# Performance work log

Measured on AMD Instinct MI355X. Metric: run time of the kernel, lower is better.

Reference implementation:

```python
import jax, jax.numpy as jnp
import numpy as np

# Model dims (match init_kwargs / input_specs)
B, CIN, COUT = 32, 32, 64
H, W = 128, 128
KH, KW = 3, 3
MAXCN = 64                    # max entries in connect_nums_list
HO, WO = H - KH + 1, W - KW + 1   # padding=0, stride=1


def setup_inputs() -> dict:
    key = jax.random.key(0)
    k1, k2, k3, k4 = jax.random.split(key, 4)
    x = jax.random.normal(k1, (B, CIN, H, W), dtype=jnp.float32)
    # padded kernel bank: [out_channel, connection_slot, kh, kw]
    weights = jax.random.normal(k2, (COUT, MAXCN, KH, KW), dtype=jnp.float32)
    # per-pixel bias map per output channel (original inits zeros; random exercises it)
    bias = jax.random.normal(k3, (COUT, HO, WO), dtype=jnp.float32) * 0.1
    connect_nums = jax.random.randint(k4, (COUT,), 1, MAXCN + 1, dtype=jnp.int32)
    return {"x": x, "weights": weights, "bias": bias, "connect_nums": connect_nums}


def reference(x, weights, bias, connect_nums):
    O, J = weights.shape[0], weights.shape[1]
    # mask out kernel slots beyond each channel's connection count
    mask = (jnp.arange(J)[None, :] < connect_nums[:, None]).astype(weights.dtype)  # [O,J]
    # slot j reads input channel j % CIN; conv is linear, so fold duplicate-channel
    # kernels into one effective dense kernel [O, CIN, KH, KW]
    onehot = jax.nn.one_hot(jnp.arange(J) % CIN, CIN, dtype=weights.dtype)  # [J,C]
    kdense = jnp.einsum('ojhw,oj,jc->ochw', weights, mask, onehot)
    out = jax.lax.conv_general_dilated(
        x, kdense, window_strides=(1, 1), padding='VALID',
        dimension_numbers=('NCHW', 'OIHW', 'NCHW'))  # [B,O,HO,WO]
    return out + bias[None]
```

## Files before the change

### kernel.cpp

```cpp
#include <hip/hip_runtime.h>

#define B_    32
#define CIN   32
#define COUT  64
#define H_    128
#define W_    128
#define HO_   126
#define WO_   126
#define MAXCN 64

typedef __attribute__((ext_vector_type(8))) short short8;
typedef __attribute__((ext_vector_type(4))) float floatx4;

static __device__ __forceinline__ unsigned short f2bf(float f) {
    union { float f; unsigned u; } v; v.f = f;
    unsigned r = v.u + 0x7fff + ((v.u >> 16) & 1);
    return (unsigned short)(r >> 16);
}

__global__ void fold_bf16(const float* __restrict__ w,
                          const int* __restrict__ cn,
                          unsigned short* __restrict__ wk) {
    int idx = blockIdx.x * 256 + threadIdx.x;
    if (idx >= 9 * COUT * CIN) return;
    int c   = idx & 31;
    int oc  = (idx >> 5) & 63;
    int tap = idx >> 11;
    int n = cn[oc];
    float v = 0.0f;
    if (c < n)      v += w[(oc * MAXCN + c) * 9 + tap];
    if (c + 32 < n) v += w[(oc * MAXCN + c + 32) * 9 + tap];
    wk[((tap * 4 + (c >> 3)) * 64 + oc) * 8 + (c & 7)] = f2bf(v);
}

__global__ __launch_bounds__(256)
void nchw_to_nhwc_bf16(const float* __restrict__ x,
                       unsigned short* __restrict__ xb) {
    const int b = blockIdx.y, y = blockIdx.x;
    const int t = threadIdx.x;
    const int c8  = t & 3;
    const int xi0 = t >> 2;
    const float* xp = x + (size_t)b * CIN * H_ * W_ + (size_t)y * W_;
#pragma unroll
    for (int it = 0; it < 2; ++it) {
        const int xi = xi0 + it * 64;
        __align__(16) unsigned short v[8];
#pragma unroll
        for (int j = 0; j < 8; ++j) {
            const int c = c8 * 8 + j;
            v[j] = f2bf(xp[(size_t)c * (H_ * W_) + xi]);
        }
        *(uint4*)(xb + (((size_t)b * H_ + y) * W_ + xi) * CIN + c8 * 8) =
            *(const uint4*)v;
    }
}

__global__ __launch_bounds__(256)
void bias_to_nhwc(const float* __restrict__ bias, float* __restrict__ bn) {
    int idx = blockIdx.x * 256 + threadIdx.x;
    int oc = idx & 63;
    int p  = idx >> 6;
    int y  = p / WO_;
    int x  = p - y * WO_;
    bn[idx] = bias[((size_t)oc * HO_ + y) * WO_ + x];
}

__global__ __launch_bounds__(256, 4)
void conv_mfma(const unsigned short* __restrict__ xb,
               const unsigned short* __restrict__ wk,
               const float* __restrict__ bnhwc,
               float* __restrict__ out) {
    const int strip = blockIdx.x;
    const int yseg  = blockIdx.y;
    const int img   = blockIdx.z;
    const int tid  = threadIdx.x;
    const int w_id = tid >> 6, lane = tid & 63;
    const int quad = lane >> 4, l16 = lane & 15;
    const int ocg  = w_id & 1;
    const int rseg = w_id >> 1;
    const int x0    = strip * 16;
    const int ybase = yseg * 16 + rseg * 8;
    const int col   = x0 + l16;
    const int colb  = col > (W_ - 3) ? (W_ - 3) : col;

    const short8* wq8 = (const short8*)wk;
    short8 a[9][2];
#pragma unroll
    for (int tap = 0; tap < 9; ++tap)
#pragma unroll
        for (int t = 0; t < 2; ++t)
            a[tap][t] = wq8[(tap * 4 + quad) * 64 + ocg * 32 + t * 16 + l16];

    const unsigned short* xbi = xb + (size_t)img * (H_ * W_ * CIN);
    float* ob = out + ((size_t)img * COUT + ocg * 32) * (HO_ * WO_);

    const int nit = (HO_ - ybase) < 8 ? (HO_ - ybase) : 8;

    for (int it = 0; it < nit; ++it) {
        const int y = ybase + it;

        const int colc = col > (WO_ - 1) ? (WO_ - 1) : col;
        const float* bp = bnhwc + ((size_t)y * WO_ + colc) * COUT + ocg * 32 + quad * 4;
        floatx4 acc[2];
        {
            const float4 b0 = *(const float4*)(bp);
            const float4 b1 = *(const float4*)(bp + 16);
            acc[0] = floatx4{b0.x, b0.y, b0.z, b0.w};
            acc[1] = floatx4{b1.x, b1.y, b1.z, b1.w};
        }

#pragma unroll
        for (int r = 0; r < 3; ++r) {
            const unsigned short* prow =
                xbi + ((size_t)(y + r) * W_ + colb) * CIN + quad * 8;
            const short8 b0 = *(const short8*)(prow);
            const short8 b1 = *(const short8*)(prow + CIN);
            const short8 b2 = *(const short8*)(prow + 2 * CIN);
            acc[0] = __builtin_amdgcn_mfma_f32_16x16x32_bf16(a[r * 3 + 0][0], b0, acc[0], 0, 0, 0);
            acc[1] = __builtin_amdgcn_mfma_f32_16x16x32_bf16(a[r * 3 + 0][1], b0, acc[1], 0, 0, 0);
            acc[0] = __builtin_amdgcn_mfma_f32_16x16x32_bf16(a[r * 3 + 1][0], b1, acc[0], 0, 0, 0);
            acc[1] = __builtin_amdgcn_mfma_f32_16x16x32_bf16(a[r * 3 + 1][1], b1, acc[1], 0, 0, 0);
            acc[0] = __builtin_amdgcn_mfma_f32_16x16x32_bf16(a[r * 3 + 2][0], b2, acc[0], 0, 0, 0);
            acc[1] = __builtin_amdgcn_mfma_f32_16x16x32_bf16(a[r * 3 + 2][1], b2, acc[1], 0, 0, 0);
        }

        if (col < WO_) {
#pragma unroll
            for (int t = 0; t < 2; ++t)
#pragma unroll
                for (int r4 = 0; r4 < 4; ++r4) {
                    const int oc_l = t * 16 + quad * 4 + r4;
                    ob[((size_t)oc_l * HO_ + y) * WO_ + col] = acc[t][r4];
                }
        }
    }
}

__global__ void fold_kernel(const float* __restrict__ w,
                            const int* __restrict__ cn,
                            float* __restrict__ kd) {
    int idx = blockIdx.x * blockDim.x + threadIdx.x;
    if (idx >= COUT * CIN * 9) return;
    int t = idx % 9;
    int c = (idx / 9) % CIN;
    int o = idx / (9 * CIN);
    int n = cn[o];
    float v = 0.0f;
    if (c < n)      v += w[(o * MAXCN + c) * 9 + t];
    if (c + 32 < n) v += w[(o * MAXCN + c + 32) * 9 + t];
    kd[idx] = v;
}

__global__ __launch_bounds__(256)
void conv_kernel(const float* __restrict__ x,
                 const float* __restrict__ kd,
                 const float* __restrict__ bias,
                 float* __restrict__ out) {
    __shared__ __align__(16) float xsh[CIN * 18 * 20];
    __shared__ __align__(16) float wsh[16 * 289];
    const int b = blockIdx.z, ocg = blockIdx.y, tile = blockIdx.x;
    const int ty = tile >> 3, txx = tile & 7;
    const int y0 = ty * 16, x0 = txx * 16;
    const int tid = threadIdx.x;
    const float* xbp = x + (size_t)b * CIN * H_ * W_;
    for (int idx = tid; idx < CIN * 18 * 18; idx += 256) {
        int c = idx / 324, rem = idx - c * 324, r = rem / 18, col = rem - r * 18;
        int iy = y0 + r;   if (iy > H_ - 1) iy = H_ - 1;
        int ix = x0 + col; if (ix > W_ - 1) ix = W_ - 1;
        xsh[c * 360 + r * 20 + col] = xbp[(c * H_ + iy) * W_ + ix];
    }
    for (int idx = tid; idx < 16 * 288; idx += 256) {
        int oc = idx / 288, rr = idx - oc * 288;
        wsh[oc * 289 + rr] = kd[(ocg * 16 + oc) * 288 + rr];
    }
    __syncthreads();
    const int oc_l = tid & 15, pb = tid >> 4, pby = pb >> 2, pbx = pb & 3;
    float acc[4][4];
#pragma unroll
    for (int i = 0; i < 4; ++i)
#pragma unroll
        for (int j = 0; j < 4; ++j) acc[i][j] = 0.0f;
    const float* xp = &xsh[(pby * 4) * 20 + pbx * 4];
    const float* wp = &wsh[oc_l * 289];
    for (int c = 0; c < CIN; ++c) {
        float xr[6][6];
#pragma unroll
        for (int r = 0; r < 6; ++r) {
            const float* row = xp + c * 360 + r * 20;
            float4 v4 = *reinterpret_cast<const float4*>(row);
            float2 v2 = *reinterpret_cast<const float2*>(row + 4);
            xr[r][0] = v4.x; xr[r][1] = v4.y; xr[r][2] = v4.z;
            xr[r][3] = v4.w; xr[r][4] = v2.x; xr[r][5] = v2.y;
        }
        float wr[9];
#pragma unroll
        for (int t = 0; t < 9; ++t) wr[t] = wp[c * 9 + t];
#pragma unroll
        for (int kh = 0; kh < 3; ++kh)
#pragma unroll
            for (int kw = 0; kw < 3; ++kw) {
                const float wv = wr[kh * 3 + kw];
#pragma unroll
                for (int i = 0; i < 4; ++i)
#pragma unroll
                    for (int j = 0; j < 4; ++j)
                        acc[i][j] = fmaf(xr[i + kh][j + kw], wv, acc[i][j]);
            }
    }
    const int o = ocg * 16 + oc_l;
    const int yb = y0 + pby * 4, xq0 = x0 + pbx * 4;
    float* ob = out + ((size_t)(b * COUT + o)) * HO_ * WO_;
    const float* bb = bias + (size_t)o * HO_ * WO_;
#pragma unroll
    for (int i = 0; i < 4; ++i) {
        int y = yb + i;
        if (y >= HO_) continue;
#pragma unroll
        for (int j = 0; j < 4; ++j) {
            int xq = xq0 + j;
            if (xq >= WO_) continue;
            ob[y * WO_ + xq] = acc[i][j] + bb[y * WO_ + xq];
        }
    }
}

extern "C" void kernel_launch(void* const* d_in, const int* in_sizes, int n_in,
                              void* d_out, int out_size, void* d_ws, size_t ws_size,
                              hipStream_t stream) {
    const float* x    = (const float*)d_in[0];
    const float* w    = (const float*)d_in[1];
    const float* bias = (const float*)d_in[2];
    const int*   cn   = (const int*)d_in[3];
    float* out = (float*)d_out;

    const size_t XB_BYTES = (size_t)B_ * H_ * W_ * CIN * 2;
    const size_t WK_BYTES = (size_t)9 * COUT * CIN * 2;
    const size_t BN_BYTES = (size_t)HO_ * WO_ * COUT * 4;

    if (ws_size >= XB_BYTES + WK_BYTES + BN_BYTES) {
        unsigned short* xbuf = (unsigned short*)d_ws;
        unsigned short* wkb  = (unsigned short*)((char*)d_ws + XB_BYTES);
        float*          bnb  = (float*)((char*)d_ws + XB_BYTES + WK_BYTES);
        fold_bf16<<<72, 256, 0, stream>>>(w, cn, wkb);
        nchw_to_nhwc_bf16<<<dim3(H_, B_), 256, 0, stream>>>(x, xbuf);
        bias_to_nhwc<<<3969, 256, 0, stream>>>(bias, bnb);
        conv_mfma<<<dim3(8, 8, B_), 256, 0, stream>>>(xbuf, wkb, bnb, out);
    } else {
        float* kd = (float*)d_ws;
        fold_kernel<<<(COUT * CIN * 9 + 255) / 256, 256, 0, stream>>>(w, cn, kd);
        dim3 grid(64, 4, B_);
        conv_kernel<<<grid, 256, 0, stream>>>(x, kd, bias, out);
    }
}
```

Measured before the change: 288.2 us.

## Reuse input rows across output rows via rolling register window; merge prep kernels

In the conv kernel, each wave now keeps a rolling window of 4 input rows in registers, so every new output row loads only one new input row instead of three. This cuts redundant global loads by roughly 3x in the main path, and the loop is fully unrolled. Separately, the weight-fold and bias-transpose kernels are merged into one launch, and the occupancy hint is lowered from 4 to 3 to leave room for the extra registers. The cost is higher register pressure, less latency hiding from occupancy, and a duplicated fallback path for partial segments.

```diff
diff --git a/kernel.cpp b/kernel.cpp
--- a/kernel.cpp
+++ b/kernel.cpp
@@ -18,19 +18,30 @@
     return (unsigned short)(r >> 16);
 }
 
-__global__ void fold_bf16(const float* __restrict__ w,
-                          const int* __restrict__ cn,
-                          unsigned short* __restrict__ wk) {
-    int idx = blockIdx.x * 256 + threadIdx.x;
-    if (idx >= 9 * COUT * CIN) return;
-    int c   = idx & 31;
-    int oc  = (idx >> 5) & 63;
-    int tap = idx >> 11;
-    int n = cn[oc];
-    float v = 0.0f;
-    if (c < n)      v += w[(oc * MAXCN + c) * 9 + tap];
-    if (c + 32 < n) v += w[(oc * MAXCN + c + 32) * 9 + tap];
-    wk[((tap * 4 + (c >> 3)) * 64 + oc) * 8 + (c & 7)] = f2bf(v);
+__global__ __launch_bounds__(256)
+void prep(const float* __restrict__ w, const int* __restrict__ cn,
+          unsigned short* __restrict__ wk,
+          const float* __restrict__ bias, float* __restrict__ bn) {
+    const int bid = blockIdx.x;
+    if (bid < 72) {
+        int idx = bid * 256 + threadIdx.x;
+        if (idx >= 9 * COUT * CIN) return;
+        int c   = idx & 31;
+        int oc  = (idx >> 5) & 63;
+        int tap = idx >> 11;
+        int n = cn[oc];
+        float v = 0.0f;
+        if (c < n)      v += w[(oc * MAXCN + c) * 9 + tap];
+        if (c + 32 < n) v += w[(oc * MAXCN + c + 32) * 9 + tap];
+        wk[((tap * 4 + (c >> 3)) * 64 + oc) * 8 + (c & 7)] = f2bf(v);
+    } else {
+        int idx = (bid - 72) * 256 + threadIdx.x;
+        int oc = idx & 63;
+        int p  = idx >> 6;
+        int y  = p / WO_;
+        int x  = p - y * WO_;
+        bn[idx] = bias[((size_t)oc * HO_ + y) * WO_ + x];
+    }
 }
 
 __global__ __launch_bounds__(256)
@@ -55,17 +66,7 @@
     }
 }
 
-__global__ __launch_bounds__(256)
-void bias_to_nhwc(const float* __restrict__ bias, float* __restrict__ bn) {
-    int idx = blockIdx.x * 256 + threadIdx.x;
-    int oc = idx & 63;
-    int p  = idx >> 6;
-    int y  = p / WO_;
-    int x  = p - y * WO_;
-    bn[idx] = bias[((size_t)oc * HO_ + y) * WO_ + x];
-}
-
-__global__ __launch_bounds__(256, 4)
+__global__ __launch_bounds__(256, 3)
 void conv_mfma(const unsigned short* __restrict__ xb,
                const unsigned short* __restrict__ wk,
                const float* __restrict__ bnhwc,
@@ -82,6 +83,7 @@
     const int ybase = yseg * 16 + rseg * 8;
     const int col   = x0 + l16;
     const int colb  = col > (W_ - 3) ? (W_ - 3) : col;
+    const int colc  = col > (WO_ - 1) ? (WO_ - 1) : col;
 
     const short8* wq8 = (const short8*)wk;
     short8 a[9][2];
@@ -90,48 +92,92 @@
 #pragma unroll
         for (int t = 0; t < 2; ++t)
             a[tap][t] = wq8[(tap * 4 + quad) * 64 + ocg * 32 + t * 16 + l16];
+#pragma unroll
+    for (int tap = 0; tap < 9; ++tap)
+#pragma unroll
+        for (int t = 0; t < 2; ++t)
+            asm volatile("" : "+v"(a[tap][t]));
 
     const unsigned short* xbi = xb + (size_t)img * (H_ * W_ * CIN);
     float* ob = out + ((size_t)img * COUT + ocg * 32) * (HO_ * WO_);
 
     const int nit = (HO_ - ybase) < 8 ? (HO_ - ybase) : 8;
 
-    for (int it = 0; it < nit; ++it) {
-        const int y = ybase + it;
-
-        const int colc = col > (WO_ - 1) ? (WO_ - 1) : col;
-        const float* bp = bnhwc + ((size_t)y * WO_ + colc) * COUT + ocg * 32 + quad * 4;
-        floatx4 acc[2];
-        {
+    if (nit == 8) {
+        short8 bw[4][3];
+#pragma unroll
+        for (int r = 0; r < 3; ++r) {
+            const unsigned short* prow =
+                xbi + ((size_t)(ybase + r) * W_ + colb) * CIN + quad * 8;
+            bw[r][0] = *(const short8*)(prow);
+            bw[r][1] = *(const short8*)(prow + CIN);
+            bw[r][2] = *(const short8*)(prow + 2 * CIN);
+        }
+#pragma unroll
+        for (int it = 0; it < 8; ++it) {
+            const int y = ybase + it;
+            if (it < 7) {
+                const unsigned short* prow =
+                    xbi + ((size_t)(y + 3) * W_ + colb) * CIN + quad * 8;
+                const int s = (it + 3) & 3;
+                bw[s][0] = *(const short8*)(prow);
+                bw[s][1] = *(const short8*)(prow + CIN);
+                bw[s][2] = *(const short8*)(prow + 2 * CIN);
+            }
+            const float* bp = bnhwc + ((size_t)y * WO_ + colc) * COUT + ocg * 32 + quad * 4;
             const float4 b0 = *(const float4*)(bp);
             const float4 b1 = *(const float4*)(bp + 16);
-            acc[0] = floatx4{b0.x, b0.y, b0.z, b0.w};
-            acc[1] = floatx4{b1.x, b1.y, b1.z, b1.w};
-        }
-
-#pragma unroll
-        for (int r = 0; r < 3; ++r) {
-            const unsigned short* prow =
-                xbi + ((size_t)(y + r) * W_ + colb) * CIN + quad * 8;
-            const short8 b0 = *(const short8*)(prow);
-            const short8 b1 = *(const short8*)(prow + CIN);
-            const short8 b2 = *(const short8*)(prow + 2 * CIN);
-            acc[0] = __builtin_amdgcn_mfma_f32_16x16x32_bf16(a[r * 3 + 0][0], b0, acc[0], 0, 0, 0);
-            acc[1] = __builtin_amdgcn_mfma_f32_16x16x32_bf16(a[r * 3 + 0][1], b0, acc[1], 0, 0, 0);
-            acc[0] = __builtin_amdgcn_mfma_f32_16x16x32_bf16(a[r * 3 + 1][0], b1, acc[0], 0, 0, 0);
-            acc[1] = __builtin_amdgcn_mfma_f32_16x16x32_bf16(a[r * 3 + 1][1], b1, acc[1], 0, 0, 0);
-            acc[0] = __builtin_amdgcn_mfma_f32_16x16x32_bf16(a[r * 3 + 2][0], b2, acc[0], 0, 0, 0);
-            acc[1] = __builtin_amdgcn_mfma_f32_16x16x32_bf16(a[r * 3 + 2][1], b2, acc[1], 0, 0, 0);
-        }
-
-        if (col < WO_) {
-#pragma unroll
-            for (int t = 0; t < 2; ++t)
+            floatx4 acc0 = floatx4{b0.x, b0.y, b0.z, b0.w};
+            floatx4 acc1 = floatx4{b1.x, b1.y, b1.z, b1.w};
+#pragma unroll
+            for (int r = 0; r < 3; ++r) {
+                const int s = (it + r) & 3;
+                acc0 = __builtin_amdgcn_mfma_f32_16x16x32_bf16(a[r * 3 + 0][0], bw[s][0], acc0, 0, 0, 0);
+                acc1 = __builtin_amdgcn_mfma_f32_16x16x32_bf16(a[r * 3 + 0][1], bw[s][0], acc1, 0, 0, 0);
+                acc0 = __builtin_amdgcn_mfma_f32_16x16x32_bf16(a[r * 3 + 1][0], bw[s][1], acc0, 0, 0, 0);
+                acc1 = __builtin_amdgcn_mfma_f32_16x16x32_bf16(a[r * 3 + 1][1], bw[s][1], acc1, 0, 0, 0);
+                acc0 = __builtin_amdgcn_mfma_f32_16x16x32_bf16(a[r * 3 + 2][0], bw[s][2], acc0, 0, 0, 0);
+                acc1 = __builtin_amdgcn_mfma_f32_16x16x32_bf16(a[r * 3 + 2][1], bw[s][2], acc1, 0, 0, 0);
+            }
+            if (col < WO_) {
 #pragma unroll
                 for (int r4 = 0; r4 < 4; ++r4) {
-                    const int oc_l = t * 16 + quad * 4 + r4;
-                    ob[((size_t)oc_l * HO_ + y) * WO_ + col] = acc[t][r4];
+                    const int o0 = quad * 4 + r4;
+                    ob[((size_t)o0 * HO_ + y) * WO_ + col] = acc0[r4];
+                    ob[((size_t)(16 + o0) * HO_ + y) * WO_ + col] = acc1[r4];
                 }
+            }
+        }
+    } else {
+        for (int it = 0; it < nit; ++it) {
+            const int y = ybase + it;
+            const float* bp = bnhwc + ((size_t)y * WO_ + colc) * COUT + ocg * 32 + quad * 4;
+            const float4 b0 = *(const float4*)(bp);
+            const float4 b1 = *(const float4*)(bp + 16);
+            floatx4 acc0 = floatx4{b0.x, b0.y, b0.z, b0.w};
+            floatx4 acc1 = floatx4{b1.x, b1.y, b1.z, b1.w};
+#pragma unroll
+            for (int r = 0; r < 3; ++r) {
+                const unsigned short* prow =
+                    xbi + ((size_t)(y + r) * W_ + colb) * CIN + quad * 8;
+                const short8 v0 = *(const short8*)(prow);
+                const short8 v1 = *(const short8*)(prow + CIN);
+                const short8 v2 = *(const short8*)(prow + 2 * CIN);
+                acc0 = __builtin_amdgcn_mfma_f32_16x16x32_bf16(a[r * 3 + 0][0], v0, acc0, 0, 0, 0);
+                acc1 = __builtin_amdgcn_mfma_f32_16x16x32_bf16(a[r * 3 + 0][1], v0, acc1, 0, 0, 0);
+                acc0 = __builtin_amdgcn_mfma_f32_16x16x32_bf16(a[r * 3 + 1][0], v1, acc0, 0, 0, 0);
+                acc1 = __builtin_amdgcn_mfma_f32_16x16x32_bf16(a[r * 3 + 1][1], v1, acc1, 0, 0, 0);
+                acc0 = __builtin_amdgcn_mfma_f32_16x16x32_bf16(a[r * 3 + 2][0], v2, acc0, 0, 0, 0);
+                acc1 = __builtin_amdgcn_mfma_f32_16x16x32_bf16(a[r * 3 + 2][1], v2, acc1, 0, 0, 0);
+            }
+            if (col < WO_) {
+#pragma unroll
+                for (int r4 = 0; r4 < 4; ++r4) {
+                    const int o0 = quad * 4 + r4;
+                    ob[((size_t)o0 * HO_ + y) * WO_ + col] = acc0[r4];
+                    ob[((size_t)(16 + o0) * HO_ + y) * WO_ + col] = acc1[r4];
+                }
+            }
         }
     }
 }
@@ -241,9 +287,8 @@
         unsigned short* xbuf = (unsigned short*)d_ws;
         unsigned short* wkb  = (unsigned short*)((char*)d_ws + XB_BYTES);
         float*          bnb  = (float*)((char*)d_ws + XB_BYTES + WK_BYTES);
-        fold_bf16<<<72, 256, 0, stream>>>(w, cn, wkb);
+        prep<<<72 + 3969, 256, 0, stream>>>(w, cn, wkb, bias, bnb);
         nchw_to_nhwc_bf16<<<dim3(H_, B_), 256, 0, stream>>>(x, xbuf);
-        bias_to_nhwc<<<3969, 256, 0, stream>>>(bias, bnb);
         conv_mfma<<<dim3(8, 8, B_), 256, 0, stream>>>(xbuf, wkb, bnb, out);
     } else {
         float* kd = (float*)d_ws;
```

Result: faster. 279.8 us (-2.9%).

## Swap MFMA operands so output lanes run along x, drop bias transpose kernel

Applied to the files above, without the earlier changes.

The MFMA operands are swapped so that pixels form the A operand and weights the B operand. Each lane's accumulator now covers 4 consecutive output x positions for a single output channel, which allows vectorized float4 stores straight into NCHW output and float4 bias loads from the original NCHW bias. This removes the separate bias_to_nhwc kernel and its workspace buffer. Blocks now cover 32x16 output tiles with 16 channels per wave, and the tile origin is clamped at the edges, so overlapping edge tiles recompute and rewrite some pixels and take a float2 path when unaligned.

```diff
diff --git a/kernel.cpp b/kernel.cpp
--- a/kernel.cpp
+++ b/kernel.cpp
@@ -56,82 +56,75 @@
 }
 
 __global__ __launch_bounds__(256)
-void bias_to_nhwc(const float* __restrict__ bias, float* __restrict__ bn) {
-    int idx = blockIdx.x * 256 + threadIdx.x;
-    int oc = idx & 63;
-    int p  = idx >> 6;
-    int y  = p / WO_;
-    int x  = p - y * WO_;
-    bn[idx] = bias[((size_t)oc * HO_ + y) * WO_ + x];
-}
-
-__global__ __launch_bounds__(256, 4)
 void conv_mfma(const unsigned short* __restrict__ xb,
                const unsigned short* __restrict__ wk,
-               const float* __restrict__ bnhwc,
+               const float* __restrict__ bias,
                float* __restrict__ out) {
     const int strip = blockIdx.x;
     const int yseg  = blockIdx.y;
     const int img   = blockIdx.z;
+    int x0 = strip * 32; if (x0 > 94) x0 = 94;
+    int y0 = yseg * 16;  if (y0 > 110) y0 = 110;
     const int tid  = threadIdx.x;
     const int w_id = tid >> 6, lane = tid & 63;
     const int quad = lane >> 4, l16 = lane & 15;
-    const int ocg  = w_id & 1;
-    const int rseg = w_id >> 1;
-    const int x0    = strip * 16;
-    const int ybase = yseg * 16 + rseg * 8;
-    const int col   = x0 + l16;
-    const int colb  = col > (W_ - 3) ? (W_ - 3) : col;
+    const int ocb  = w_id * 16;
 
     const short8* wq8 = (const short8*)wk;
-    short8 a[9][2];
+    short8 wfrag[9];
 #pragma unroll
     for (int tap = 0; tap < 9; ++tap)
-#pragma unroll
-        for (int t = 0; t < 2; ++t)
-            a[tap][t] = wq8[(tap * 4 + quad) * 64 + ocg * 32 + t * 16 + l16];
+        wfrag[tap] = wq8[(tap * 4 + quad) * 64 + ocb + l16];
+#pragma unroll
+    for (int tap = 0; tap < 9; ++tap)
+        asm volatile("" : "+v"(wfrag[tap]));
 
     const unsigned short* xbi = xb + (size_t)img * (H_ * W_ * CIN);
-    float* ob = out + ((size_t)img * COUT + ocg * 32) * (HO_ * WO_);
-
-    const int nit = (HO_ - ybase) < 8 ? (HO_ - ybase) : 8;
-
-    for (int it = 0; it < nit; ++it) {
-        const int y = ybase + it;
-
-        const int colc = col > (WO_ - 1) ? (WO_ - 1) : col;
-        const float* bp = bnhwc + ((size_t)y * WO_ + colc) * COUT + ocg * 32 + quad * 4;
-        floatx4 acc[2];
-        {
+    const float* bp0 = bias + ((size_t)(ocb + l16) * HO_ + y0) * WO_ + x0 + quad * 4;
+    float* op0 = out + (((size_t)(img * COUT + ocb + l16)) * HO_ + y0) * WO_ + x0 + quad * 4;
+    const bool aligned = (x0 & 3) == 0;
+
+    for (int it = 0; it < 16; ++it) {
+        const int y = y0 + it;
+        const float* bp = bp0 + it * WO_;
+        float* op = op0 + it * WO_;
+
+        floatx4 acc0, acc1;
+        if (aligned) {
             const float4 b0 = *(const float4*)(bp);
             const float4 b1 = *(const float4*)(bp + 16);
-            acc[0] = floatx4{b0.x, b0.y, b0.z, b0.w};
-            acc[1] = floatx4{b1.x, b1.y, b1.z, b1.w};
+            acc0 = floatx4{b0.x, b0.y, b0.z, b0.w};
+            acc1 = floatx4{b1.x, b1.y, b1.z, b1.w};
+        } else {
+            const float2 b0a = *(const float2*)(bp);
+            const float2 b0b = *(const float2*)(bp + 2);
+            const float2 b1a = *(const float2*)(bp + 16);
+            const float2 b1b = *(const float2*)(bp + 18);
+            acc0 = floatx4{b0a.x, b0a.y, b0b.x, b0b.y};
+            acc1 = floatx4{b1a.x, b1a.y, b1b.x, b1b.y};
         }
 
 #pragma unroll
         for (int r = 0; r < 3; ++r) {
             const unsigned short* prow =
-                xbi + ((size_t)(y + r) * W_ + colb) * CIN + quad * 8;
-            const short8 b0 = *(const short8*)(prow);
-            const short8 b1 = *(const short8*)(prow + CIN);
-            const short8 b2 = *(const short8*)(prow + 2 * CIN);
-            acc[0] = __builtin_amdgcn_mfma_f32_16x16x32_bf16(a[r * 3 + 0][0], b0, acc[0], 0, 0, 0);
-            acc[1] = __builtin_amdgcn_mfma_f32_16x16x32_bf16(a[r * 3 + 0][1], b0, acc[1], 0, 0, 0);
-            acc[0] = __builtin_amdgcn_mfma_f32_16x16x32_bf16(a[r * 3 + 1][0], b1, acc[0], 0, 0, 0);
-            acc[1] = __builtin_amdgcn_mfma_f32_16x16x32_bf16(a[r * 3 + 1][1], b1, acc[1], 0, 0, 0);
-            acc[0] = __builtin_amdgcn_mfma_f32_16x16x32_bf16(a[r * 3 + 2][0], b2, acc[0], 0, 0, 0);
-            acc[1] = __builtin_amdgcn_mfma_f32_16x16x32_bf16(a[r * 3 + 2][1], b2, acc[1], 0, 0, 0);
-        }
-
-        if (col < WO_) {
-#pragma unroll
-            for (int t = 0; t < 2; ++t)
-#pragma unroll
-                for (int r4 = 0; r4 < 4; ++r4) {
-                    const int oc_l = t * 16 + quad * 4 + r4;
-                    ob[((size_t)oc_l * HO_ + y) * WO_ + col] = acc[t][r4];
-                }
+                xbi + ((size_t)(y + r) * W_ + x0 + l16) * CIN + quad * 8;
+#pragma unroll
+            for (int kw = 0; kw < 3; ++kw) {
+                const short8 p0 = *(const short8*)(prow + kw * CIN);
+                const short8 p1 = *(const short8*)(prow + (16 + kw) * CIN);
+                acc0 = __builtin_amdgcn_mfma_f32_16x16x32_bf16(p0, wfrag[r * 3 + kw], acc0, 0, 0, 0);
+                acc1 = __builtin_amdgcn_mfma_f32_16x16x32_bf16(p1, wfrag[r * 3 + kw], acc1, 0, 0, 0);
+            }
+        }
+
+        if (aligned) {
+            *(floatx4*)(op)      = acc0;
+            *(floatx4*)(op + 16) = acc1;
+        } else {
+            *(float2*)(op)      = float2{acc0[0], acc0[1]};
+            *(float2*)(op + 2)  = float2{acc0[2], acc0[3]};
+            *(float2*)(op + 16) = float2{acc1[0], acc1[1]};
+            *(float2*)(op + 18) = float2{acc1[2], acc1[3]};
         }
     }
 }
@@ -235,16 +228,13 @@
 
     const size_t XB_BYTES = (size_t)B_ * H_ * W_ * CIN * 2;
     const size_t WK_BYTES = (size_t)9 * COUT * CIN * 2;
-    const size_t BN_BYTES = (size_t)HO_ * WO_ * COUT * 4;
-
-    if (ws_size >= XB_BYTES + WK_BYTES + BN_BYTES) {
+
+    if (ws_size >= XB_BYTES + WK_BYTES) {
         unsigned short* xbuf = (unsigned short*)d_ws;
         unsigned short* wkb  = (unsigned short*)((char*)d_ws + XB_BYTES);
-        float*          bnb  = (float*)((char*)d_ws + XB_BYTES + WK_BYTES);
         fold_bf16<<<72, 256, 0, stream>>>(w, cn, wkb);
         nchw_to_nhwc_bf16<<<dim3(H_, B_), 256, 0, stream>>>(x, xbuf);
-        bias_to_nhwc<<<3969, 256, 0, stream>>>(bias, bnb);
-        conv_mfma<<<dim3(8, 8, B_), 256, 0, stream>>>(xbuf, wkb, bnb, out);
+        conv_mfma<<<dim3(4, 8, B_), 256, 0, stream>>>(xbuf, wkb, bias, out);
     } else {
         float* kd = (float*)d_ws;
         fold_kernel<<<(COUT * CIN * 9 + 255) / 256, 256, 0, stream>>>(w, cn, kd);
```

Measured after the change: 273.8 us. -5.0%, faster.
